# Performance work log

Measured on AMD Instinct MI355X. Metric: run time of the kernel, lower is better.

Reference implementation:

```python
import jax, jax.numpy as jnp
import numpy as np

B, IN, OUT = 8192, 4096, 4096

def setup_inputs() -> dict:
    key = jax.random.key(0)
    k1, k2, k3 = jax.random.split(key, 3)
    x = jax.random.normal(k1, (B, IN), dtype=jnp.float32)
    # nn.Linear default init: U(-1/sqrt(in), 1/sqrt(in))
    bound = 1.0 / np.sqrt(IN)
    W = jax.random.uniform(k2, (OUT, IN), dtype=jnp.float32, minval=-bound, maxval=bound)
    b = jax.random.uniform(k3, (OUT,), dtype=jnp.float32, minval=-bound, maxval=bound)
    return {"x": x, "W": W, "b": b}

def reference(x, W, b):
    # L2-normalize each row (eps added to norm, matching torch)
    norm = jnp.sqrt(jnp.sum(x * x, axis=1, keepdims=True))
    x_n = x / (norm + 1e-8)
    # Linear: y = x_n @ W^T + b, then ReLU
    y = jnp.einsum('bi,oi->bo', x_n, W) + b
    return jax.nn.relu(y)
```

## Files before the change

### kernel.cpp

```cpp
#include <hip/hip_runtime.h>
#include <hip/hip_bf16.h>
#include <cstdint>
#include <cstddef>

#define GLB(p)  ((const __attribute__((address_space(1))) void*)(p))
#define LDSP(p) ((__attribute__((address_space(3))) void*)(p))

typedef __attribute__((ext_vector_type(8))) __bf16 bf16x8;
typedef __attribute__((ext_vector_type(4))) float  f32x4;
typedef __attribute__((ext_vector_type(8))) unsigned short u16x8;

static constexpr int Mdim = 8192, Ndim = 4096, Kdim = 4096;

#define S_BAR()      do { asm volatile("" ::: "memory"); __builtin_amdgcn_s_barrier(); asm volatile("" ::: "memory"); } while (0)
#define WAIT_LGKM(n) asm volatile("s_waitcnt lgkmcnt(" #n ")" ::: "memory")
#define WAIT_VM(n)   asm volatile("s_waitcnt vmcnt(" #n ")" ::: "memory")

static __device__ __forceinline__ unsigned short f2bf_bits(float f) {
    __hip_bfloat16 h = __float2bfloat16(f);
    return __builtin_bit_cast(unsigned short, h);
}

static __device__ __forceinline__ int swz16k(int p) {
    return p ^ (((p >> 7) & 7) << 4);
}

__global__ void __launch_bounds__(256) preproc_kernel(const float* __restrict__ x,
                                                      const float* __restrict__ Wf,
                                                      __hip_bfloat16* __restrict__ xn,
                                                      __hip_bfloat16* __restrict__ Wb)
{
    const int row = blockIdx.x;
    const int t = threadIdx.x;

    const float4* xr = (const float4*)(x + (size_t)row * Kdim);
    float4 v[4];
    float s = 0.f;
#pragma unroll
    for (int i = 0; i < 4; ++i) {
        v[i] = xr[i * 256 + t];
        s += v[i].x * v[i].x + v[i].y * v[i].y + v[i].z * v[i].z + v[i].w * v[i].w;
    }
#pragma unroll
    for (int off = 32; off > 0; off >>= 1) s += __shfl_down(s, off, 64);
    __shared__ float red[4];
    const int lane = t & 63, w = t >> 6;
    if (lane == 0) red[w] = s;
    __syncthreads();
    const float tot = red[0] + red[1] + red[2] + red[3];
    const float inv = 1.f / (sqrtf(tot) + 1e-8f);
    ushort4* xo = (ushort4*)(xn + (size_t)row * Kdim);
#pragma unroll
    for (int i = 0; i < 4; ++i) {
        ushort4 o;
        o.x = f2bf_bits(v[i].x * inv);
        o.y = f2bf_bits(v[i].y * inv);
        o.z = f2bf_bits(v[i].z * inv);
        o.w = f2bf_bits(v[i].w * inv);
        xo[i * 256 + t] = o;
    }

    const size_t idx = (size_t)row * 256 + t;
    const float4* p = (const float4*)Wf + idx * 2;
    const float4 a = p[0], c = p[1];
    u16x8 o;
    o[0] = f2bf_bits(a.x); o[1] = f2bf_bits(a.y);
    o[2] = f2bf_bits(a.z); o[3] = f2bf_bits(a.w);
    o[4] = f2bf_bits(c.x); o[5] = f2bf_bits(c.y);
    o[6] = f2bf_bits(c.z); o[7] = f2bf_bits(c.w);
    *((u16x8*)Wb + idx) = o;
}

__global__ void __launch_bounds__(512, 2) gemm256_8p(
        const __hip_bfloat16* __restrict__ A,
        const __hip_bfloat16* __restrict__ B,
        const float* __restrict__ bias,
        float* __restrict__ out)
{
    constexpr int NT  = Kdim / 64;
    constexpr int NTN = Ndim / 256;
    constexpr int NWG = (Mdim / 256) * NTN;
    extern __shared__ char smem[];

    const int bid = blockIdx.x;
    const int swz = (bid & 7) * (NWG / 8) + (bid >> 3);
    const int m0 = (swz / NTN) * 256;
    const int n0 = (swz % NTN) * 256;

    const int tid  = threadIdx.x;
    const int lane = tid & 63;
    const int w    = tid >> 6;
    const int wm   = w >> 2;
    const int wn   = w & 3;
    const int fr   = lane & 15;
    const int ko2  = (lane >> 4) * 16;
    const int xm   = (lane & 7) << 4;
    const int brow = (wn & 1) * 64;

    const int p0 = tid * 16;
    const int p1 = 8192 + tid * 16;
    const int q0 = swz16k(p0);
    const int q1 = swz16k(p1);
    const int sr0 = q0 >> 7, sc0 = (q0 & 127) >> 1;
    const int sr1 = q1 >> 7, sc1 = (q1 & 127) >> 1;

    const __hip_bfloat16* Ab0 = A + (size_t)(m0 + sr0) * Kdim + sc0;
    const __hip_bfloat16* Ab1 = A + (size_t)(m0 + sr1) * Kdim + sc1;
    const __hip_bfloat16* Bb0 = B + (size_t)(n0 + sr0) * Kdim + sc0;
    const __hip_bfloat16* Bb1 = B + (size_t)(n0 + sr1) * Kdim + sc1;

#define STAGE_A(tt, h) do { \
        char* ld_ = smem + ((2 * (tt) + (h)) & 3) * 16384; \
        __builtin_amdgcn_global_load_lds(GLB(Ab0 + (size_t)(h) * (128 * Kdim) + (tt) * 64), LDSP(ld_ + p0), 16, 0, 0); \
        __builtin_amdgcn_global_load_lds(GLB(Ab1 + (size_t)(h) * (128 * Kdim) + (tt) * 64), LDSP(ld_ + p1), 16, 0, 0); \
    } while (0)
#define STAGE_B(tt, h) do { \
        char* ld_ = smem + 65536 + ((2 * (tt) + (h)) & 3) * 16384; \
        __builtin_amdgcn_global_load_lds(GLB(Bb0 + (size_t)(h) * (128 * Kdim) + (tt) * 64), LDSP(ld_ + p0), 16, 0, 0); \
        __builtin_amdgcn_global_load_lds(GLB(Bb1 + (size_t)(h) * (128 * Kdim) + (tt) * 64), LDSP(ld_ + p1), 16, 0, 0); \
    } while (0)

#define LDS_RD(base, row, kb) (*(const bf16x8*)(smem + ((((base) + (row) * 128 + (kb))) ^ xm)))

#define A_RD(buf, m) do { \
        buf[0] = LDS_RD(sa, (m) * 16 + fr, ko2); \
        buf[1] = LDS_RD(sa, (m) * 16 + fr, 64 + ko2); } while (0)

#define MFMA8(m, buf) do { \
    __builtin_amdgcn_s_setprio(1); \
    _Pragma("unroll") for (int kk = 0; kk < 2; ++kk) \
    _Pragma("unroll") for (int j = 0; j < 4; ++j) \
        acc[(m)][j] = __builtin_amdgcn_mfma_f32_16x16x32_bf16(buf[kk], bfr[j][kk], acc[(m)][j], 0, 0, 0); \
    __builtin_amdgcn_s_setprio(0); } while (0)

    f32x4 acc[8][4];
#pragma unroll
    for (int i = 0; i < 8; ++i)
#pragma unroll
        for (int j = 0; j < 4; ++j) acc[i][j] = (f32x4){0.f, 0.f, 0.f, 0.f};

    bf16x8 aA[2], aB[2], bfr[4][2];

    STAGE_A(0, 0); STAGE_A(0, 1); STAGE_B(0, 0); STAGE_B(0, 1);
    STAGE_A(1, 0); STAGE_A(1, 1);
    WAIT_VM(4);
    S_BAR();

#pragma unroll 2
    for (int t = 0; t < NT; ++t) {
        const int sa = ((2 * t + wm) & 3) * 16384;
        const int sb = 65536 + ((2 * t + (wn >> 1)) & 3) * 16384;
        const int tb = (t + 1) & (NT - 1);
        const int ta = (t + 2) & (NT - 1);

#pragma unroll
        for (int j = 0; j < 4; ++j) {
            bfr[j][0] = LDS_RD(sb, brow + j * 16 + fr, ko2);
            bfr[j][1] = LDS_RD(sb, brow + j * 16 + fr, 64 + ko2);
        }
        A_RD(aA, 0);
        STAGE_B(tb, 0); STAGE_B(tb, 1);

        A_RD(aB, 1); MFMA8(0, aA);
        A_RD(aA, 2); MFMA8(1, aB);
        A_RD(aB, 3); MFMA8(2, aA);
        A_RD(aA, 4); MFMA8(3, aB);
        A_RD(aB, 5); MFMA8(4, aA);
        A_RD(aA, 6); MFMA8(5, aB);
        A_RD(aB, 7); MFMA8(6, aA);

        WAIT_LGKM(0);
        S_BAR();
        STAGE_A(ta, 0); STAGE_A(ta, 1);
        MFMA8(7, aB);
        WAIT_VM(4);
        S_BAR();
    }
    WAIT_VM(0);

#undef STAGE_A
#undef STAGE_B
#undef LDS_RD
#undef A_RD
#undef MFMA8

    const int cl = lane & 15;
    const int rl = (lane >> 4) * 4;
#pragma unroll
    for (int j = 0; j < 4; ++j) {
        const int col = n0 + wn * 64 + j * 16 + cl;
        const float bv = bias[col];
#pragma unroll
        for (int i = 0; i < 8; ++i) {
            const int row = m0 + wm * 128 + i * 16 + rl;
            float* po = out + (size_t)row * Ndim + col;
#pragma unroll
            for (int q = 0; q < 4; ++q) {
                const float r = acc[i][j][q] + bv;
                po[(size_t)q * Ndim] = r > 0.f ? r : 0.f;
            }
        }
    }
}

__global__ void __launch_bounds__(256) gemm_bias_relu_kernel(
        const __hip_bfloat16* __restrict__ A,
        const __hip_bfloat16* __restrict__ B,
        const float* __restrict__ bias,
        float* __restrict__ out)
{
    constexpr int BM = 128, BN = 128, BK = 32;
    constexpr int NT_N = Ndim / BN;
    constexpr int NWG  = (Mdim / BM) * NT_N;

    __shared__ __bf16 As[BM * BK];
    __shared__ __bf16 Bs[BN * BK];

    const int bid = blockIdx.x;
    const int swz = (bid & 7) * (NWG / 8) + (bid >> 3);
    const int by = swz / NT_N, bx = swz % NT_N;
    const int m0 = by * BM, n0 = bx * BN;

    const int tid  = threadIdx.x;
    const int lane = tid & 63;
    const int w    = tid >> 6;
    const int wm   = w >> 1, wn = w & 1;

    const int o0 = w * 1024 + lane * 16;
    const int o1 = o0 + 4096;
    const int r0 = o0 >> 6, e0 = (o0 & 63) >> 1;
    const int r1 = o1 >> 6, e1 = (o1 & 63) >> 1;

    const __hip_bfloat16* a0 = A + (size_t)(m0 + r0) * Kdim + e0;
    const __hip_bfloat16* a1 = A + (size_t)(m0 + r1) * Kdim + e1;
    const __hip_bfloat16* b0 = B + (size_t)(n0 + r0) * Kdim + e0;
    const __hip_bfloat16* b1 = B + (size_t)(n0 + r1) * Kdim + e1;
    __bf16* lA0 = As + (o0 >> 1);
    __bf16* lA1 = As + (o1 >> 1);
    __bf16* lB0 = Bs + (o0 >> 1);
    __bf16* lB1 = Bs + (o1 >> 1);

    f32x4 acc[4][4];
#pragma unroll
    for (int i = 0; i < 4; ++i)
#pragma unroll
        for (int j = 0; j < 4; ++j) acc[i][j] = (f32x4){0.f, 0.f, 0.f, 0.f};

    const int fr = lane & 15;
    const int ko = (lane >> 4) * 8;

    for (int kt = 0; kt < Kdim; kt += BK) {
        __builtin_amdgcn_global_load_lds(GLB(a0 + kt), LDSP(lA0), 16, 0, 0);
        __builtin_amdgcn_global_load_lds(GLB(a1 + kt), LDSP(lA1), 16, 0, 0);
        __builtin_amdgcn_global_load_lds(GLB(b0 + kt), LDSP(lB0), 16, 0, 0);
        __builtin_amdgcn_global_load_lds(GLB(b1 + kt), LDSP(lB1), 16, 0, 0);
        __syncthreads();

        bf16x8 af[4], bfr[4];
#pragma unroll
        for (int i = 0; i < 4; ++i)
            af[i]  = *(const bf16x8*)&As[(wm * 64 + i * 16 + fr) * BK + ko];
#pragma unroll
        for (int j = 0; j < 4; ++j)
            bfr[j] = *(const bf16x8*)&Bs[(wn * 64 + j * 16 + fr) * BK + ko];

#pragma unroll
        for (int i = 0; i < 4; ++i)
#pragma unroll
            for (int j = 0; j < 4; ++j)
                acc[i][j] = __builtin_amdgcn_mfma_f32_16x16x32_bf16(af[i], bfr[j], acc[i][j], 0, 0, 0);
        __syncthreads();
    }

    const int cl = lane & 15;
    const int rl = (lane >> 4) * 4;
#pragma unroll
    for (int j = 0; j < 4; ++j) {
        const int col = n0 + wn * 64 + j * 16 + cl;
        const float bv = bias[col];
#pragma unroll
        for (int i = 0; i < 4; ++i) {
            const int row = m0 + wm * 64 + i * 16 + rl;
            float* po = out + (size_t)row * Ndim + col;
#pragma unroll
            for (int q = 0; q < 4; ++q) {
                const float r = acc[i][j][q] + bv;
                po[(size_t)q * Ndim] = r > 0.f ? r : 0.f;
            }
        }
    }
}

__global__ void __launch_bounds__(256) rownorm_only_kernel(const float* __restrict__ x,
                                                           float* __restrict__ invn)
{
    const int row = blockIdx.x;
    const int t = threadIdx.x;
    const float4* xr = (const float4*)(x + (size_t)row * Kdim);
    float s = 0.f;
#pragma unroll
    for (int i = 0; i < 4; ++i) {
        const float4 v = xr[i * 256 + t];
        s += v.x * v.x + v.y * v.y + v.z * v.z + v.w * v.w;
    }
#pragma unroll
    for (int off = 32; off > 0; off >>= 1) s += __shfl_down(s, off, 64);
    __shared__ float red[4];
    if ((t & 63) == 0) red[t >> 6] = s;
    __syncthreads();
    if (t == 0) {
        const float tot = red[0] + red[1] + red[2] + red[3];
        invn[row] = 1.f / (sqrtf(tot) + 1e-8f);
    }
}

__global__ void __launch_bounds__(256) fallback_gemm_kernel(
        const float* __restrict__ x, const float* __restrict__ W,
        const float* __restrict__ b, const float* __restrict__ invn,
        float* __restrict__ out)
{
    __shared__ float At[16][17], Bt[16][17];
    const int tx = threadIdx.x & 15, ty = threadIdx.x >> 4;
    const int m = blockIdx.y * 16 + ty;
    const int n = blockIdx.x * 16 + tx;
    float s = 0.f;
    for (int k0 = 0; k0 < Kdim; k0 += 16) {
        At[ty][tx] = x[(size_t)m * Kdim + k0 + tx];
        Bt[ty][tx] = W[(size_t)(blockIdx.x * 16 + ty) * Kdim + k0 + tx];
        __syncthreads();
#pragma unroll
        for (int kk = 0; kk < 16; ++kk) s += At[ty][kk] * Bt[tx][kk];
        __syncthreads();
    }
    s = s * invn[m] + b[n];
    out[(size_t)m * Ndim + n] = s > 0.f ? s : 0.f;
}

extern "C" void kernel_launch(void* const* d_in, const int* in_sizes, int n_in,
                              void* d_out, int out_size, void* d_ws, size_t ws_size,
                              hipStream_t stream)
{
    (void)in_sizes; (void)n_in; (void)out_size;
    const float* x = (const float*)d_in[0];
    const float* W = (const float*)d_in[1];
    const float* b = (const float*)d_in[2];
    float* out = (float*)d_out;

    const size_t needA = (size_t)Mdim * Kdim * sizeof(__hip_bfloat16);
    const size_t needW = (size_t)Ndim * Kdim * sizeof(__hip_bfloat16);

    if (ws_size >= needA + needW) {
        __hip_bfloat16* Xn = (__hip_bfloat16*)d_ws;
        __hip_bfloat16* Wb = (__hip_bfloat16*)((char*)d_ws + needA);
        preproc_kernel<<<Mdim, 256, 0, stream>>>(x, W, Xn, Wb);

        hipError_t e = hipFuncSetAttribute((const void*)gemm256_8p,
                                           hipFuncAttributeMaxDynamicSharedMemorySize,
                                           131072);
        if (e == hipSuccess) {
            gemm256_8p<<<(Mdim / 256) * (Ndim / 256), 512, 131072, stream>>>(Xn, Wb, b, out);
        } else {
            gemm_bias_relu_kernel<<<(Mdim / 128) * (Ndim / 128), 256, 0, stream>>>(Xn, Wb, b, out);
        }
    } else {
        float* invn = (float*)d_ws;
        rownorm_only_kernel<<<Mdim, 256, 0, stream>>>(x, invn);
        dim3 g(Ndim / 16, Mdim / 16);
        fallback_gemm_kernel<<<g, 256, 0, stream>>>(x, W, b, invn, out);
    }
}
```

Baseline: 282.8 us.

## Load B fragments directly from global into double-buffered registers, bypassing LDS

The GEMM no longer stages the W (B) tile through LDS. Each wave now loads its B MFMA fragments straight from global memory into registers, double-buffered across two k-tiles, with the loop manually unrolled by two to alternate the buffers. This halves the dynamic LDS to 64KB and removes the B LDS reads. In exchange, each wave issues narrow, partly strided global loads, waves sharing the same B columns load the same data twice, and register pressure rises. The B load latency is hidden by only one tile of compute.

```diff
diff --git a/kernel.cpp b/kernel.cpp
--- a/kernel.cpp
+++ b/kernel.cpp
@@ -71,7 +71,7 @@
     *((u16x8*)Wb + idx) = o;
 }
 
-__global__ void __launch_bounds__(512, 2) gemm256_8p(
+__global__ void __launch_bounds__(512, 2) gemm256_bd(
         const __hip_bfloat16* __restrict__ A,
         const __hip_bfloat16* __restrict__ B,
         const float* __restrict__ bias,
@@ -95,7 +95,6 @@
     const int fr   = lane & 15;
     const int ko2  = (lane >> 4) * 16;
     const int xm   = (lane & 7) << 4;
-    const int brow = (wn & 1) * 64;
 
     const int p0 = tid * 16;
     const int p1 = 8192 + tid * 16;
@@ -106,19 +105,19 @@
 
     const __hip_bfloat16* Ab0 = A + (size_t)(m0 + sr0) * Kdim + sc0;
     const __hip_bfloat16* Ab1 = A + (size_t)(m0 + sr1) * Kdim + sc1;
-    const __hip_bfloat16* Bb0 = B + (size_t)(n0 + sr0) * Kdim + sc0;
-    const __hip_bfloat16* Bb1 = B + (size_t)(n0 + sr1) * Kdim + sc1;
+    const __hip_bfloat16* Bg = B + (size_t)(n0 + wn * 64 + fr) * Kdim + ((lane >> 4) * 8);
 
 #define STAGE_A(tt, h) do { \
         char* ld_ = smem + ((2 * (tt) + (h)) & 3) * 16384; \
         __builtin_amdgcn_global_load_lds(GLB(Ab0 + (size_t)(h) * (128 * Kdim) + (tt) * 64), LDSP(ld_ + p0), 16, 0, 0); \
         __builtin_amdgcn_global_load_lds(GLB(Ab1 + (size_t)(h) * (128 * Kdim) + (tt) * 64), LDSP(ld_ + p1), 16, 0, 0); \
     } while (0)
-#define STAGE_B(tt, h) do { \
-        char* ld_ = smem + 65536 + ((2 * (tt) + (h)) & 3) * 16384; \
-        __builtin_amdgcn_global_load_lds(GLB(Bb0 + (size_t)(h) * (128 * Kdim) + (tt) * 64), LDSP(ld_ + p0), 16, 0, 0); \
-        __builtin_amdgcn_global_load_lds(GLB(Bb1 + (size_t)(h) * (128 * Kdim) + (tt) * 64), LDSP(ld_ + p1), 16, 0, 0); \
-    } while (0)
+
+#define B_LOAD(dst, tt) do { \
+    _Pragma("unroll") for (int j = 0; j < 4; ++j) { \
+        dst[j][0] = *(const bf16x8*)(Bg + (size_t)j * (16 * Kdim) + (tt) * 64); \
+        dst[j][1] = *(const bf16x8*)(Bg + (size_t)j * (16 * Kdim) + (tt) * 64 + 32); \
+    } } while (0)
 
 #define LDS_RD(base, row, kb) (*(const bf16x8*)(smem + ((((base) + (row) * 128 + (kb))) ^ xm)))
 
@@ -126,63 +125,59 @@
         buf[0] = LDS_RD(sa, (m) * 16 + fr, ko2); \
         buf[1] = LDS_RD(sa, (m) * 16 + fr, 64 + ko2); } while (0)
 
-#define MFMA8(m, buf) do { \
+#define MFMA8(m, abuf, bset) do { \
     __builtin_amdgcn_s_setprio(1); \
     _Pragma("unroll") for (int kk = 0; kk < 2; ++kk) \
     _Pragma("unroll") for (int j = 0; j < 4; ++j) \
-        acc[(m)][j] = __builtin_amdgcn_mfma_f32_16x16x32_bf16(buf[kk], bfr[j][kk], acc[(m)][j], 0, 0, 0); \
+        acc[(m)][j] = __builtin_amdgcn_mfma_f32_16x16x32_bf16(abuf[kk], bset[j][kk], acc[(m)][j], 0, 0, 0); \
     __builtin_amdgcn_s_setprio(0); } while (0)
 
+#define TILE_BODY(t, bcur, bnext) do { \
+        const int sa = ((2 * (t) + wm) & 3) * 16384; \
+        const int ta = ((t) + 2) & (NT - 1); \
+        B_LOAD(bnext, ((t) + 1) & (NT - 1)); \
+        A_RD(aA, 0); \
+        A_RD(aB, 1); MFMA8(0, aA, bcur); \
+        A_RD(aA, 2); MFMA8(1, aB, bcur); \
+        A_RD(aB, 3); MFMA8(2, aA, bcur); \
+        A_RD(aA, 4); MFMA8(3, aB, bcur); \
+        A_RD(aB, 5); MFMA8(4, aA, bcur); \
+        A_RD(aA, 6); MFMA8(5, aB, bcur); \
+        A_RD(aB, 7); MFMA8(6, aA, bcur); \
+        WAIT_LGKM(0); \
+        S_BAR();                                \
+        STAGE_A(ta, 0); STAGE_A(ta, 1); \
+        MFMA8(7, aB, bcur); \
+        WAIT_VM(4);                             \
+        S_BAR(); \
+    } while (0)
+
     f32x4 acc[8][4];
 #pragma unroll
     for (int i = 0; i < 8; ++i)
 #pragma unroll
         for (int j = 0; j < 4; ++j) acc[i][j] = (f32x4){0.f, 0.f, 0.f, 0.f};
 
-    bf16x8 aA[2], aB[2], bfr[4][2];
-
-    STAGE_A(0, 0); STAGE_A(0, 1); STAGE_B(0, 0); STAGE_B(0, 1);
+    bf16x8 aA[2], aB[2], bf0[4][2], bf1[4][2];
+
+    B_LOAD(bf0, 0);
+    STAGE_A(0, 0); STAGE_A(0, 1);
     STAGE_A(1, 0); STAGE_A(1, 1);
     WAIT_VM(4);
     S_BAR();
 
-#pragma unroll 2
-    for (int t = 0; t < NT; ++t) {
-        const int sa = ((2 * t + wm) & 3) * 16384;
-        const int sb = 65536 + ((2 * t + (wn >> 1)) & 3) * 16384;
-        const int tb = (t + 1) & (NT - 1);
-        const int ta = (t + 2) & (NT - 1);
-
-#pragma unroll
-        for (int j = 0; j < 4; ++j) {
-            bfr[j][0] = LDS_RD(sb, brow + j * 16 + fr, ko2);
-            bfr[j][1] = LDS_RD(sb, brow + j * 16 + fr, 64 + ko2);
-        }
-        A_RD(aA, 0);
-        STAGE_B(tb, 0); STAGE_B(tb, 1);
-
-        A_RD(aB, 1); MFMA8(0, aA);
-        A_RD(aA, 2); MFMA8(1, aB);
-        A_RD(aB, 3); MFMA8(2, aA);
-        A_RD(aA, 4); MFMA8(3, aB);
-        A_RD(aB, 5); MFMA8(4, aA);
-        A_RD(aA, 6); MFMA8(5, aB);
-        A_RD(aB, 7); MFMA8(6, aA);
-
-        WAIT_LGKM(0);
-        S_BAR();
-        STAGE_A(ta, 0); STAGE_A(ta, 1);
-        MFMA8(7, aB);
-        WAIT_VM(4);
-        S_BAR();
+    for (int t = 0; t < NT; t += 2) {
+        TILE_BODY(t,     bf0, bf1);
+        TILE_BODY(t + 1, bf1, bf0);
     }
     WAIT_VM(0);
 
 #undef STAGE_A
-#undef STAGE_B
+#undef B_LOAD
 #undef LDS_RD
 #undef A_RD
 #undef MFMA8
+#undef TILE_BODY
 
     const int cl = lane & 15;
     const int rl = (lane >> 4) * 4;
@@ -354,11 +349,11 @@
         __hip_bfloat16* Wb = (__hip_bfloat16*)((char*)d_ws + needA);
         preproc_kernel<<<Mdim, 256, 0, stream>>>(x, W, Xn, Wb);
 
-        hipError_t e = hipFuncSetAttribute((const void*)gemm256_8p,
+        hipError_t e = hipFuncSetAttribute((const void*)gemm256_bd,
                                            hipFuncAttributeMaxDynamicSharedMemorySize,
-                                           131072);
+                                           65536);
         if (e == hipSuccess) {
-            gemm256_8p<<<(Mdim / 256) * (Ndim / 256), 512, 131072, stream>>>(Xn, Wb, b, out);
+            gemm256_bd<<<(Mdim / 256) * (Ndim / 256), 512, 65536, stream>>>(Xn, Wb, b, out);
         } else {
             gemm_bias_relu_kernel<<<(Mdim / 128) * (Ndim / 128), 256, 0, stream>>>(Xn, Wb, b, out);
         }
```

After: 419.1 us. 48.2% more time.
